# Optimization experiments

Hardware: AMD Instinct MI355X
Metric: run time of the kernel (lower is better)

The kernel has to match this reference:

```python
import jax, jax.numpy as jnp
import numpy as np

B, N, DF = 8, 4096, 768
K1, K2, DS = 8, 2, 128
KVQ, H, ITERS = 128, 1, 3
DH = KVQ // H
EPS_SA = 1e-8
SCALE = DH ** -0.5


def layer_norm(x, g, b, eps=1e-5):
    m = jnp.mean(x, axis=-1, keepdims=True)
    v = jnp.var(x, axis=-1, keepdims=True)
    return (x - m) / jnp.sqrt(v + eps) * g + b


def gru_cell(x, h, Wih, Whh, bih, bhh):
    gi = x @ Wih.T + bih
    gh = h @ Whh.T + bhh
    ir, iz, inn = jnp.split(gi, 3, axis=-1)
    hr, hz, hn = jnp.split(gh, 3, axis=-1)
    r = jax.nn.sigmoid(ir + hr)
    z = jax.nn.sigmoid(iz + hz)
    n = jnp.tanh(inn + r * hn)
    return (1.0 - z) * n + z * h


def setup_inputs() -> dict:
    key = jax.random.key(0)
    ks = jax.random.split(key, 24)
    s = 0.02
    f32 = jnp.float32
    return {
        'tokens': jax.random.normal(ks[0], (B, N, DF), f32),
        'parent_slots': jax.random.normal(ks[1], (B, K1, DS), f32),
        'parent_masks': jax.random.uniform(ks[2], (B, K1, N), f32),
        'eps_noise': jax.random.normal(ks[3], (B, K1, K2, DS), f32),
        'ln_in_g': jnp.ones((DF,), f32), 'ln_in_b': jnp.zeros((DF,), f32),
        'ln_s_g': jnp.ones((DS,), f32), 'ln_s_b': jnp.zeros((DS,), f32),
        'Wq': jax.random.normal(ks[4], (KVQ, DS), f32) * s,
        'Wk': jax.random.normal(ks[5], (KVQ, DF), f32) * s,
        'Wv': jax.random.normal(ks[6], (KVQ, DF), f32) * s,
        'gru_Wih': jax.random.normal(ks[7], (3 * DS, KVQ), f32) * s,
        'gru_Whh': jax.random.normal(ks[8], (3 * DS, DS), f32) * s,
        'gru_bih': jnp.zeros((3 * DS,), f32),
        'gru_bhh': jnp.zeros((3 * DS,), f32),
        'mlp_ln_g': jnp.ones((DS,), f32), 'mlp_ln_b': jnp.zeros((DS,), f32),
        'mlp_W1': jax.random.normal(ks[9], (4 * DS, DS), f32) * s,
        'mlp_b1': jnp.zeros((4 * DS,), f32),
        'mlp_W2': jax.random.normal(ks[10], (DS, 4 * DS), f32) * s,
        'mlp_b2': jnp.zeros((DS,), f32),
    }


def reference(tokens, parent_slots, parent_masks, eps_noise,
              ln_in_g, ln_in_b, ln_s_g, ln_s_b, Wq, Wk, Wv,
              gru_Wih, gru_Whh, gru_bih, gru_bhh,
              mlp_ln_g, mlp_ln_b, mlp_W1, mlp_b1, mlp_W2, mlp_b2):
    BK = B * K1
    # parent-mask gating (all parents vectorized, folded into batch)
    denom = jnp.mean(parent_masks, axis=-1, keepdims=True)          # [B,K1,1]
    safe = (denom > 1e-6).astype(tokens.dtype)
    w_scaled = safe * (parent_masks / (denom + 1e-6)) + (1.0 - safe)  # [B,K1,N]
    tg = (tokens[:, None, :, :] * w_scaled[..., None]).reshape(BK, N, DF)
    slots = (parent_slots[:, :, None, :] + 0.01 * eps_noise).reshape(BK, K2, DS)

    inp = layer_norm(tg, ln_in_g, ln_in_b)
    k = (inp @ Wk.T).reshape(BK, N, H, DH)
    v = (inp @ Wv.T).reshape(BK, N, H, DH)

    attn_bw = None
    for _ in range(ITERS):
        slots_prev = slots
        sn = layer_norm(slots, ln_s_g, ln_s_b)
        q = (sn @ Wq.T).reshape(BK, K2, H, DH)
        dots = jnp.einsum('bihd,bjhd->bihj', q, k) * SCALE          # [BK,K2,H,N]
        attn = jax.nn.softmax(dots, axis=1) + EPS_SA                # softmax over slots
        attn_bw = attn
        attn_w = attn / jnp.sum(attn, axis=-1, keepdims=True)
        updates = jnp.einsum('bjhd,bihj->bihd', v, attn_w).reshape(BK * K2, KVQ)
        slots = gru_cell(updates, slots_prev.reshape(BK * K2, DS),
                         gru_Wih, gru_Whh, gru_bih, gru_bhh).reshape(BK, K2, DS)
        h = layer_norm(slots, mlp_ln_g, mlp_ln_b)
        slots = jax.nn.gelu(h @ mlp_W1.T + mlp_b1, approximate=False) @ mlp_W2.T + mlp_b2

    attn_out = jnp.mean(attn_bw, axis=2)                            # [BK,K2,N]
    child_objects = slots.reshape(B, K1 * K2, DS)
    child_gating = (attn_out.reshape(B, K1, K2, N) * parent_masks[:, :, None, :]).reshape(B, K1 * K2, N)
    return child_objects, child_gating
```

## Files before the change

### kernel.cpp

```cpp
#include <hip/hip_runtime.h>
#include <math.h>

#define SCALE_ 0.08838834764831843f

typedef __attribute__((ext_vector_type(8))) short bf16x8;
typedef __attribute__((ext_vector_type(4))) float f32x4;
typedef __attribute__((ext_vector_type(8))) unsigned short u16x8;

static const size_t OFF_VAR   = 0;
static const size_t OFF_DENOM = 32768;
static const size_t OFF_GSUM  = 32832;
static const size_t OFF_BIAS  = 33088;
static const size_t OFF_QKB   = 33344;
static const size_t OFF_SSUM  = 33472;
static const size_t OFF_SLOTS = 33600;
static const size_t OFF_Q     = 49984;
static const size_t OFF_U     = 66368;
static const size_t OFF_WQBF  = 82752;
static const size_t OFF_WIHBF = 90944;
static const size_t OFF_WHHBF = 115520;
static const size_t OFF_W1BF  = 140096;
static const size_t OFF_WM2BF = 172864;
static const size_t OFF_WKVBF = 205632;
static const size_t OFF_KVB   = 303936;

__device__ __forceinline__ float wred64(float v) {
#pragma unroll
  for (int off = 32; off > 0; off >>= 1) v += __shfl_xor(v, off, 64);
  return v;
}

__device__ __forceinline__ unsigned short f2bf(float f) {
  unsigned u = __float_as_uint(f);
  unsigned r = (u + 0x7fffu + ((u >> 16) & 1u)) >> 16;
  return (unsigned short)r;
}

__device__ __forceinline__ unsigned pack2(float a, float b) {
  return (unsigned)f2bf(a) | ((unsigned)f2bf(b) << 16);
}

__device__ __forceinline__ float bf2f(unsigned short s) {
  return __uint_as_float((unsigned)s << 16);
}

__global__ __launch_bounds__(256) void prep_all_k(
    const float* __restrict__ Wk, const float* __restrict__ Wv,
    const float* __restrict__ g, const float* __restrict__ bb,
    const float* __restrict__ Wq, const float* __restrict__ Wih,
    const float* __restrict__ Whh, const float* __restrict__ W1,
    const float* __restrict__ W2, const float* __restrict__ pm,
    unsigned short* __restrict__ wkv, float* __restrict__ gsum,
    float* __restrict__ biasArr,
    unsigned short* __restrict__ Wqbf, unsigned short* __restrict__ Wihbf,
    unsigned short* __restrict__ Whhbf, unsigned short* __restrict__ W1bf,
    unsigned short* __restrict__ Wm2bf, float* __restrict__ denomArr)
{
  __shared__ float red4[4];
  int bi = blockIdx.x, t = threadIdx.x;
  if (bi < 64) {
    int j = bi*4 + (t >> 6), lane = t & 63;
    const float* w = (j < 128) ? (Wk + (size_t)j*768) : (Wv + (size_t)(j-128)*768);
    float gs = 0.f, bs = 0.f;
    int key = j & 7;
#pragma unroll
    for (int s = 0; s < 12; ++s) {
      int dd = lane + s*64;
      float wv = w[dd], gv = g[dd];
      gs += gv*wv; bs += bb[dd]*wv;
      int sw = (dd & ~63) | (((((dd >> 3) & 7) ^ key)) << 3) | (dd & 7);
      wkv[(size_t)j*768 + sw] = f2bf(wv*gv);
    }
    gs = wred64(gs); bs = wred64(bs);
    if (lane == 0) { gsum[j] = gs; biasArr[j] = bs; }
  } else if (bi < 128) {
    int idx = (bi-64)*256 + t;  Wqbf[idx]  = f2bf(Wq[idx]);
  } else if (bi < 320) {
    int idx = (bi-128)*256 + t; Wihbf[idx] = f2bf(Wih[idx]);
  } else if (bi < 512) {
    int idx = (bi-320)*256 + t; Whhbf[idx] = f2bf(Whh[idx]);
  } else if (bi < 768) {
    int idx = (bi-512)*256 + t; W1bf[idx]  = f2bf(W1[idx]);
  } else if (bi < 1024) {
    int idx = (bi-768)*256 + t; Wm2bf[idx] = f2bf(W2[idx]);
  } else {
    int bk = bi - 1024;
    float s = 0.f;
#pragma unroll
    for (int k = 0; k < 16; ++k) s += pm[bk*4096 + t + k*256];
    s = wred64(s);
    if ((t & 63) == 0) red4[t >> 6] = s;
    __syncthreads();
    if (t == 0) denomArr[bk] = (red4[0]+red4[1]+red4[2]+red4[3])*(1.f/4096.f);
  }
}

__global__ __launch_bounds__(256) void gemm_kv_k(
    const float* __restrict__ tokens, const unsigned short* __restrict__ wkv,
    const float* __restrict__ gsum, unsigned short* __restrict__ KVb,
    float* __restrict__ varArr)
{
  __shared__ unsigned short As[64*64];
  __shared__ unsigned short Bs[256*64];
  __shared__ float meanS[64];
  int r0 = blockIdx.x*64;
  int t = threadIdx.x;
  int w = t >> 6, lane = t & 63;
  int lm = lane & 15, lq = lane >> 4;
  int g16 = t >> 4, seg = t & 15;
  int m0 = (w >> 1)*32, n0 = (w & 1)*128;

  f32x4 acc[2][8];
#pragma unroll
  for (int a = 0; a < 2; ++a)
#pragma unroll
    for (int c = 0; c < 8; ++c) acc[a][c] = f32x4{0.f, 0.f, 0.f, 0.f};
  float s1[4] = {0.f,0.f,0.f,0.f}, s2[4] = {0.f,0.f,0.f,0.f};

  for (int k0 = 0; k0 < 768; k0 += 64) {
    __syncthreads();
#pragma unroll
    for (int s = 0; s < 8; ++s) {
      int row = w*64 + s*8;
      __builtin_amdgcn_global_load_lds(
        (const __attribute__((address_space(1))) void*)
          (wkv + (size_t)(row + (lane >> 3))*768 + k0 + (lane & 7)*8),
        (__attribute__((address_space(3))) void*)(&Bs[row*64]), 16, 0, 0);
    }
#pragma unroll
    for (int p = 0; p < 4; ++p) {
      int row = p*16 + g16;
      float4 x = *(const float4*)(tokens + (size_t)(r0 + row)*768 + k0 + seg*4);
      s1[p] += x.x + x.y + x.z + x.w;
      s2[p] += x.x*x.x + x.y*x.y + x.z*x.z + x.w*x.w;
      int off = row*64 + (((seg >> 1) ^ (row & 7)) << 3) + (seg & 1)*4;
      *(uint2*)(&As[off]) = make_uint2(pack2(x.x, x.y), pack2(x.z, x.w));
    }
    __syncthreads();
#pragma unroll
    for (int kk8 = 0; kk8 < 8; kk8 += 4) {
      bf16x8 af[2], bfr[8];
#pragma unroll
      for (int mt = 0; mt < 2; ++mt) {
        int row = m0 + mt*16 + lm;
        af[mt] = *(const bf16x8*)(&As[row*64 + (((kk8 + lq) ^ (row & 7)) << 3)]);
      }
#pragma unroll
      for (int nt = 0; nt < 8; ++nt) {
        int row = n0 + nt*16 + lm;
        bfr[nt] = *(const bf16x8*)(&Bs[row*64 + (((kk8 + lq) ^ (row & 7)) << 3)]);
      }
#pragma unroll
      for (int mt = 0; mt < 2; ++mt)
#pragma unroll
        for (int nt = 0; nt < 8; ++nt)
          acc[mt][nt] = __builtin_amdgcn_mfma_f32_16x16x32_bf16(
              af[mt], bfr[nt], acc[mt][nt], 0, 0, 0);
    }
  }
#pragma unroll
  for (int p = 0; p < 4; ++p) {
#pragma unroll
    for (int m = 8; m >= 1; m >>= 1) {
      s1[p] += __shfl_xor(s1[p], m, 16);
      s2[p] += __shfl_xor(s2[p], m, 16);
    }
  }
  if (seg == 0) {
#pragma unroll
    for (int p = 0; p < 4; ++p) {
      int row = p*16 + g16;
      float m = s1[p]*(1.f/768.f);
      meanS[row] = m;
      varArr[r0 + row] = s2[p]*(1.f/768.f) - m*m;
    }
  }
  __syncthreads();
#pragma unroll
  for (int nt = 0; nt < 8; ++nt) {
    int jg = n0 + nt*16 + lm;
    float gs = gsum[jg];
#pragma unroll
    for (int mt = 0; mt < 2; ++mt) {
#pragma unroll
      for (int reg = 0; reg < 4; ++reg) {
        int rl = m0 + mt*16 + lq*4 + reg;
        KVb[(size_t)(r0 + rl)*256 + jg] = f2bf(acc[mt][nt][reg] - meanS[rl]*gs);
      }
    }
  }
}

__global__ __launch_bounds__(256, 1) void slots_init_q_k(
    const float* __restrict__ ps, const float* __restrict__ eps,
    const float* __restrict__ g_s, const float* __restrict__ b_s,
    const unsigned short* __restrict__ Wqbf, const float* __restrict__ biasArr,
    float* __restrict__ slots, float* __restrict__ qg, float* __restrict__ qkb,
    float* __restrict__ Ssum, float* __restrict__ U)
{
  __shared__ unsigned short Fsn[2048];
  __shared__ float qkbL[16];
  int R0 = blockIdx.x*16;
  int t = threadIdx.x;
  int w = t >> 6, ln = t & 63, lm = ln & 15, lq = ln >> 4;
  if (t < 16) qkbL[t] = 0.f;
  {
    int r = t >> 4, dseg = t & 15, ds8 = dseg*8;
    int row = R0 + r, bk = row >> 1;
    float xv[8]; float s1 = 0.f, s2 = 0.f;
#pragma unroll
    for (int j = 0; j < 8; ++j) {
      int d = ds8 + j;
      float x = ps[bk*128 + d] + 0.01f*eps[row*128 + d];
      slots[row*128 + d] = x;
      U[row*128 + d] = 0.f;
      xv[j] = x; s1 += x; s2 += x*x;
    }
#pragma unroll
    for (int m = 8; m >= 1; m >>= 1) {
      s1 += __shfl_xor(s1, m, 16);
      s2 += __shfl_xor(s2, m, 16);
    }
    float mean = s1*(1.f/128.f);
    float var = s2*(1.f/128.f) - mean*mean;
    float rstd = rsqrtf(var + 1e-5f);
    float sv[8];
#pragma unroll
    for (int j = 0; j < 8; ++j) {
      int d = ds8 + j;
      sv[j] = (xv[j] - mean)*rstd*g_s[d] + b_s[d];
    }
    int fa = ((dseg >> 2)*64 + (dseg & 3)*16 + r)*8;
    *(uint4*)&Fsn[fa] = make_uint4(pack2(sv[0],sv[1]), pack2(sv[2],sv[3]),
                                   pack2(sv[4],sv[5]), pack2(sv[6],sv[7]));
  }
  __syncthreads();
  {
    bf16x8 af[4];
#pragma unroll
    for (int kc = 0; kc < 4; ++kc)
      af[kc] = *(const bf16x8*)(&Fsn[(kc*64 + ln)*8]);
    float pr[4] = {0.f, 0.f, 0.f, 0.f};
#pragma unroll
    for (int i = 0; i < 2; ++i) {
      int n0 = w*32 + i*16;
      f32x4 acc = f32x4{0.f,0.f,0.f,0.f};
#pragma unroll
      for (int kc = 0; kc < 4; ++kc) {
        bf16x8 bw = *(const bf16x8*)(&Wqbf[(size_t)(n0+lm)*128 + kc*32 + lq*8]);
        acc = __builtin_amdgcn_mfma_f32_16x16x32_bf16(af[kc], bw, acc, 0,0,0);
      }
      int n = n0 + lm;
      float bk_ = biasArr[n];
#pragma unroll
      for (int reg = 0; reg < 4; ++reg) {
        int row = lq*4 + reg;
        qg[(size_t)(R0 + row)*128 + n] = acc[reg];
        pr[reg] += acc[reg]*bk_;
      }
    }
#pragma unroll
    for (int reg = 0; reg < 4; ++reg) {
#pragma unroll
      for (int m = 8; m >= 1; m >>= 1) pr[reg] += __shfl_xor(pr[reg], m, 16);
    }
    if (lm == 0) {
#pragma unroll
      for (int reg = 0; reg < 4; ++reg)
        atomicAdd(&qkbL[lq*4 + reg], pr[reg]);
    }
  }
  __syncthreads();
  if (t < 16) { qkb[R0 + t] = qkbL[t]; Ssum[R0 + t] = 0.f; }
}

__global__ __launch_bounds__(256) void attn_fused_k(
    const unsigned short* __restrict__ KVb, const float* __restrict__ qg,
    const float* __restrict__ qkb, const float* __restrict__ varArr,
    const float* __restrict__ denomArr, const float* __restrict__ pm,
    float* __restrict__ U, float* __restrict__ Ssum,
    float* __restrict__ outG, int last)
{
  __shared__ float KVs[32*260];
  __shared__ float qs[2048];
  __shared__ float was[16*33];
  __shared__ float qkbs[16];
  int bi = blockIdx.x;
  int b = bi & 7, ch = bi >> 3;
  int t = threadIdx.x;
#pragma unroll
  for (int s = 0; s < 2; ++s)
    ((float4*)qs)[s*256 + t] = ((const float4*)(qg + b*2048))[s*256 + t];
  if (t < 16) qkbs[t] = qkb[b*16 + t];
  int p = t >> 5, nl = t & 31;
  int iu = t >> 4, dg = t & 15;
  int bk = b*8 + p;
  float den = denomArr[bk];
  float acc8[8];
#pragma unroll
  for (int j = 0; j < 8; ++j) acc8[j] = 0.f;
  float sA0 = 0.f, sA1 = 0.f;
  const float* q0 = qs + (p*2)*128;
  const float* q1 = q0 + 128;
  __syncthreads();
  float qb0 = qkbs[p*2], qb1 = qkbs[p*2 + 1];
  for (int sub = 0; sub < 4; ++sub) {
    int n0 = ch*128 + sub*32;
    if (sub) __syncthreads();
    {
      int nn = t >> 3, jj = t & 7;
#pragma unroll
      for (int s = 0; s < 4; ++s) {
        int col8 = jj + s*8;
        u16x8 kv8 = *(const u16x8*)&KVb[((size_t)(b*4096 + n0 + nn))*256 + col8*8];
        float4 f0, f1;
        f0.x = bf2f(kv8[0]); f0.y = bf2f(kv8[1]); f0.z = bf2f(kv8[2]); f0.w = bf2f(kv8[3]);
        f1.x = bf2f(kv8[4]); f1.y = bf2f(kv8[5]); f1.z = bf2f(kv8[6]); f1.w = bf2f(kv8[7]);
        *(float4*)&KVs[nn*260 + col8*8] = f0;
        *(float4*)&KVs[nn*260 + col8*8 + 4] = f1;
      }
    }
    __syncthreads();
    float d0 = 0.f, d1 = 0.f;
    const float* kr = KVs + nl*260;
#pragma unroll 8
    for (int j4 = 0; j4 < 32; ++j4) {
      float4 kv = *(const float4*)(kr + j4*4);
      float4 qa = *(const float4*)(q0 + j4*4);
      float4 qb = *(const float4*)(q1 + j4*4);
      d0 += kv.x*qa.x + kv.y*qa.y + kv.z*qa.z + kv.w*qa.w;
      d1 += kv.x*qb.x + kv.y*qb.y + kv.z*qb.z + kv.w*qb.w;
    }
    int n = n0 + nl;
    float pmv = pm[(size_t)bk*4096 + n];
    float c = (den > 1e-6f) ? (pmv/(den + 1e-6f)) : 1.f;
    float vv = varArr[b*4096 + n];
    float al = c*rsqrtf(c*c*vv + 1e-5f);
    float dd0 = SCALE_*(al*d0 + qb0);
    float dd1 = SCALE_*(al*d1 + qb1);
    float mx = fmaxf(dd0, dd1);
    float e0 = expf(dd0 - mx), e1 = expf(dd1 - mx);
    float inv = 1.f/(e0 + e1);
    float o0 = e0*inv + 1e-8f;
    float o1 = e1*inv + 1e-8f;
    sA0 += o0; sA1 += o1;
    was[(p*2)*33 + nl] = o0*al;
    was[(p*2 + 1)*33 + nl] = o1*al;
    if (last) {
      outG[((size_t)(bk*2))*4096 + n] = o0*pmv;
      outG[((size_t)(bk*2 + 1))*4096 + n] = o1*pmv;
    }
    __syncthreads();
    const float* vb = KVs + 128 + dg*8;
    const float* wr = was + iu*33;
#pragma unroll 8
    for (int nn = 0; nn < 32; ++nn) {
      float wv = wr[nn];
      float4 v0 = *(const float4*)(vb + nn*260);
      float4 v1 = *(const float4*)(vb + nn*260 + 4);
      acc8[0] += wv*v0.x; acc8[1] += wv*v0.y; acc8[2] += wv*v0.z; acc8[3] += wv*v0.w;
      acc8[4] += wv*v1.x; acc8[5] += wv*v1.y; acc8[6] += wv*v1.z; acc8[7] += wv*v1.w;
    }
  }
#pragma unroll
  for (int m = 16; m >= 1; m >>= 1) {
    sA0 += __shfl_xor(sA0, m, 32);
    sA1 += __shfl_xor(sA1, m, 32);
  }
  if (nl == 0) {
    atomicAdd(&Ssum[bk*2], sA0);
    atomicAdd(&Ssum[bk*2 + 1], sA1);
  }
  float* ur = U + (size_t)(b*16 + iu)*128 + dg*8;
#pragma unroll
  for (int j = 0; j < 8; ++j) atomicAdd(ur + j, acc8[j]);
}

__global__ __launch_bounds__(256, 1) void gru_mlp_q_k(
    const float* __restrict__ Uin, const float* __restrict__ Ssum,
    const float* __restrict__ biasArr,
    const unsigned short* __restrict__ Wihbf, const unsigned short* __restrict__ Whhbf,
    const float* __restrict__ bih, const float* __restrict__ bhh,
    const float* __restrict__ mlp_g, const float* __restrict__ mlp_b,
    const unsigned short* __restrict__ W1bf, const float* __restrict__ b1,
    const unsigned short* __restrict__ Wm2bf, const float* __restrict__ b2,
    const float* __restrict__ ln_s_g, const float* __restrict__ ln_s_b,
    const unsigned short* __restrict__ Wqbf,
    float* __restrict__ slots, float* __restrict__ qg, float* __restrict__ qkb,
    float* __restrict__ SsumW, float* __restrict__ Uw,
    float* __restrict__ outObj, int last)
{
  __shared__ unsigned short FXx[2048], FXh[2048], Fhn[2048], Fsn[2048];
  __shared__ unsigned short Ft1[8192];
  __shared__ float G_rz[16*256];
  __shared__ float G_in[16*128];
  __shared__ float G_hn[16*128];
  __shared__ float hs_[16*128];
  __shared__ float os_[16*128];
  __shared__ float qkbL[16];

  int R0 = blockIdx.x*16;
  int t = threadIdx.x;
  int w = t >> 6, ln = t & 63;
  int lm = ln & 15, lq = ln >> 4;

  {
    int r = t >> 4, dseg = t & 15, ds8 = dseg*8;
    int R = R0 + r;
    const float* up = Uin + (size_t)R*128 + ds8;
    float4 u0 = *(const float4*)(up);
    float4 u1 = *(const float4*)(up + 4);
    float Sv = 1.f/Ssum[R];
    float4 bv0 = *(const float4*)(biasArr + 128 + ds8);
    float4 bv1 = *(const float4*)(biasArr + 132 + ds8);
    float xv[8];
    xv[0]=u0.x*Sv+bv0.x; xv[1]=u0.y*Sv+bv0.y; xv[2]=u0.z*Sv+bv0.z; xv[3]=u0.w*Sv+bv0.w;
    xv[4]=u1.x*Sv+bv1.x; xv[5]=u1.y*Sv+bv1.y; xv[6]=u1.z*Sv+bv1.z; xv[7]=u1.w*Sv+bv1.w;
    if (!last) {
      *(float4*)(Uw + (size_t)R*128 + ds8) = make_float4(0.f,0.f,0.f,0.f);
      *(float4*)(Uw + (size_t)R*128 + ds8 + 4) = make_float4(0.f,0.f,0.f,0.f);
    }
    float4 h0 = *(const float4*)(slots + (size_t)R*128 + ds8);
    float4 h1 = *(const float4*)(slots + (size_t)R*128 + ds8 + 4);
    *(float4*)(hs_ + r*128 + ds8) = h0;
    *(float4*)(hs_ + r*128 + ds8 + 4) = h1;
    int fa = ((dseg >> 2)*64 + (dseg & 3)*16 + r)*8;
    *(uint4*)&FXx[fa] = make_uint4(pack2(xv[0],xv[1]), pack2(xv[2],xv[3]),
                                   pack2(xv[4],xv[5]), pack2(xv[6],xv[7]));
    *(uint4*)&FXh[fa] = make_uint4(pack2(h0.x,h0.y), pack2(h0.z,h0.w),
                                   pack2(h1.x,h1.y), pack2(h1.z,h1.w));
    if (t < 16) qkbL[t] = 0.f;
  }
  __syncthreads();

  {
    bf16x8 ax[4], ah[4];
#pragma unroll
    for (int kc = 0; kc < 4; ++kc) {
      ax[kc] = *(const bf16x8*)(&FXx[(kc*64 + ln)*8]);
      ah[kc] = *(const bf16x8*)(&FXh[(kc*64 + ln)*8]);
    }
    if (w < 2) {
#pragma unroll
      for (int i = 0; i < 8; ++i) {
        int n0 = (w*8 + i)*16;
        f32x4 acc = f32x4{0.f,0.f,0.f,0.f};
#pragma unroll
        for (int kc = 0; kc < 4; ++kc) {
          bf16x8 bi_ = *(const bf16x8*)(&Wihbf[(size_t)(n0+lm)*128 + kc*32 + lq*8]);
          acc = __builtin_amdgcn_mfma_f32_16x16x32_bf16(ax[kc], bi_, acc, 0,0,0);
        }
#pragma unroll
        for (int kc = 0; kc < 4; ++kc) {
          bf16x8 bh_ = *(const bf16x8*)(&Whhbf[(size_t)(n0+lm)*128 + kc*32 + lq*8]);
          acc = __builtin_amdgcn_mfma_f32_16x16x32_bf16(ah[kc], bh_, acc, 0,0,0);
        }
#pragma unroll
        for (int reg = 0; reg < 4; ++reg)
          G_rz[(lq*4+reg)*256 + n0 + lm] = acc[reg];
      }
    } else if (w == 2) {
#pragma unroll
      for (int i = 0; i < 8; ++i) {
        int n0 = 256 + i*16;
        f32x4 acc = f32x4{0.f,0.f,0.f,0.f};
#pragma unroll
        for (int kc = 0; kc < 4; ++kc) {
          bf16x8 bi_ = *(const bf16x8*)(&Wihbf[(size_t)(n0+lm)*128 + kc*32 + lq*8]);
          acc = __builtin_amdgcn_mfma_f32_16x16x32_bf16(ax[kc], bi_, acc, 0,0,0);
        }
#pragma unroll
        for (int reg = 0; reg < 4; ++reg)
          G_in[(lq*4+reg)*128 + i*16 + lm] = acc[reg];
      }
    } else {
#pragma unroll
      for (int i = 0; i < 8; ++i) {
        int n0 = 256 + i*16;
        f32x4 acc = f32x4{0.f,0.f,0.f,0.f};
#pragma unroll
        for (int kc = 0; kc < 4; ++kc) {
          bf16x8 bh_ = *(const bf16x8*)(&Whhbf[(size_t)(n0+lm)*128 + kc*32 + lq*8]);
          acc = __builtin_amdgcn_mfma_f32_16x16x32_bf16(ah[kc], bh_, acc, 0,0,0);
        }
#pragma unroll
        for (int reg = 0; reg < 4; ++reg)
          G_hn[(lq*4+reg)*128 + i*16 + lm] = acc[reg];
      }
    }
  }
  __syncthreads();

  {
    int r = t >> 4, dseg = t & 15, ds8 = dseg*8;
    float hp[8];
    float s1 = 0.f, s2 = 0.f;
#pragma unroll
    for (int j = 0; j < 8; ++j) {
      int d = ds8 + j;
      float rg = G_rz[r*256 + d] + bih[d] + bhh[d];
      float zg = G_rz[r*256 + 128 + d] + bih[128+d] + bhh[128+d];
      float ing = G_in[r*128 + d] + bih[256+d];
      float hng = G_hn[r*128 + d] + bhh[256+d];
      float rv = 1.f/(1.f + expf(-rg));
      float zv = 1.f/(1.f + expf(-zg));
      float nv = tanhf(ing + rv*hng);
      float h0 = hs_[r*128 + d];
      float h = (1.f - zv)*nv + zv*h0;
      hp[j] = h;
      s1 += h; s2 += h*h;
    }
#pragma unroll
    for (int m = 8; m >= 1; m >>= 1) {
      s1 += __shfl_xor(s1, m, 16);
      s2 += __shfl_xor(s2, m, 16);
    }
    float mean = s1*(1.f/128.f);
    float var = s2*(1.f/128.f) - mean*mean;
    float rstd = rsqrtf(var + 1e-5f);
    float hv[8];
#pragma unroll
    for (int j = 0; j < 8; ++j) {
      int d = ds8 + j;
      hv[j] = (hp[j] - mean)*rstd*mlp_g[d] + mlp_b[d];
    }
    int fa = ((dseg >> 2)*64 + (dseg & 3)*16 + r)*8;
    *(uint4*)&Fhn[fa] = make_uint4(pack2(hv[0],hv[1]), pack2(hv[2],hv[3]),
                                   pack2(hv[4],hv[5]), pack2(hv[6],hv[7]));
  }
  __syncthreads();

  {
    bf16x8 af[4];
#pragma unroll
    for (int kc = 0; kc < 4; ++kc)
      af[kc] = *(const bf16x8*)(&Fhn[(kc*64 + ln)*8]);
#pragma unroll
    for (int i = 0; i < 8; ++i) {
      int n0 = (w*8 + i)*16;
      f32x4 acc = f32x4{0.f,0.f,0.f,0.f};
#pragma unroll
      for (int kc = 0; kc < 4; ++kc) {
        bf16x8 bw = *(const bf16x8*)(&W1bf[(size_t)(n0+lm)*128 + kc*32 + lq*8]);
        acc = __builtin_amdgcn_mfma_f32_16x16x32_bf16(af[kc], bw, acc, 0,0,0);
      }
      int kdim = n0 + lm;
      float bb = b1[kdim];
      int kc2 = kdim >> 5;
      int sub = (kdim >> 3) & 3;
      int jj = kdim & 7;
#pragma unroll
      for (int reg = 0; reg < 4; ++reg) {
        float v = acc[reg] + bb;
        float gel = 0.5f*v*(1.f + erff(v*0.70710678118654752f));
        Ft1[(kc2*64 + sub*16 + lq*4 + reg)*8 + jj] = f2bf(gel);
      }
    }
  }
  __syncthreads();

  {
#pragma unroll
    for (int i = 0; i < 2; ++i) {
      int n0 = w*32 + i*16;
      f32x4 acc = f32x4{0.f,0.f,0.f,0.f};
#pragma unroll
      for (int kc = 0; kc < 16; ++kc) {
        bf16x8 af = *(const bf16x8*)(&Ft1[(kc*64 + ln)*8]);
        bf16x8 bw = *(const bf16x8*)(&Wm2bf[(size_t)(n0+lm)*512 + kc*32 + lq*8]);
        acc = __builtin_amdgcn_mfma_f32_16x16x32_bf16(af, bw, acc, 0,0,0);
      }
      int n = n0 + lm;
      float bb = b2[n];
#pragma unroll
      for (int reg = 0; reg < 4; ++reg) {
        int row = lq*4 + reg;
        float o = acc[reg] + bb;
        slots[(size_t)(R0 + row)*128 + n] = o;
        os_[row*128 + n] = o;
        if (last) outObj[(size_t)(R0 + row)*128 + n] = o;
      }
    }
  }

  if (last) return;

  __syncthreads();
  {
    int r = t >> 4, dseg = t & 15, ds8 = dseg*8;
    float ov[8];
    float s1 = 0.f, s2 = 0.f;
#pragma unroll
    for (int j = 0; j < 8; ++j) {
      float o = os_[r*128 + ds8 + j];
      ov[j] = o; s1 += o; s2 += o*o;
    }
#pragma unroll
    for (int m = 8; m >= 1; m >>= 1) {
      s1 += __shfl_xor(s1, m, 16);
      s2 += __shfl_xor(s2, m, 16);
    }
    float mean = s1*(1.f/128.f);
    float var = s2*(1.f/128.f) - mean*mean;
    float rstd = rsqrtf(var + 1e-5f);
    float sv[8];
#pragma unroll
    for (int j = 0; j < 8; ++j) {
      int d = ds8 + j;
      sv[j] = (ov[j] - mean)*rstd*ln_s_g[d] + ln_s_b[d];
    }
    int fa = ((dseg >> 2)*64 + (dseg & 3)*16 + r)*8;
    *(uint4*)&Fsn[fa] = make_uint4(pack2(sv[0],sv[1]), pack2(sv[2],sv[3]),
                                   pack2(sv[4],sv[5]), pack2(sv[6],sv[7]));
  }
  __syncthreads();

  {
    bf16x8 af[4];
#pragma unroll
    for (int kc = 0; kc < 4; ++kc)
      af[kc] = *(const bf16x8*)(&Fsn[(kc*64 + ln)*8]);
    float pr[4] = {0.f, 0.f, 0.f, 0.f};
#pragma unroll
    for (int i = 0; i < 2; ++i) {
      int n0 = w*32 + i*16;
      f32x4 acc = f32x4{0.f,0.f,0.f,0.f};
#pragma unroll
      for (int kc = 0; kc < 4; ++kc) {
        bf16x8 bw = *(const bf16x8*)(&Wqbf[(size_t)(n0+lm)*128 + kc*32 + lq*8]);
        acc = __builtin_amdgcn_mfma_f32_16x16x32_bf16(af[kc], bw, acc, 0,0,0);
      }
      int n = n0 + lm;
      float bk_ = biasArr[n];
#pragma unroll
      for (int reg = 0; reg < 4; ++reg) {
        int row = lq*4 + reg;
        qg[(size_t)(R0 + row)*128 + n] = acc[reg];
        pr[reg] += acc[reg]*bk_;
      }
    }
#pragma unroll
    for (int reg = 0; reg < 4; ++reg) {
#pragma unroll
      for (int m = 8; m >= 1; m >>= 1) pr[reg] += __shfl_xor(pr[reg], m, 16);
    }
    if (lm == 0) {
#pragma unroll
      for (int reg = 0; reg < 4; ++reg)
        atomicAdd(&qkbL[lq*4 + reg], pr[reg]);
    }
  }
  __syncthreads();
  if (t < 16) {
    qkb[R0 + t] = qkbL[t];
    SsumW[R0 + t] = 0.f;
  }
}

extern "C" void kernel_launch(void* const* d_in, const int* in_sizes, int n_in,
                              void* d_out, int out_size, void* d_ws, size_t ws_size,
                              hipStream_t stream) {
  const float* tokens = (const float*)d_in[0];
  const float* pslots = (const float*)d_in[1];
  const float* pmasks = (const float*)d_in[2];
  const float* eps    = (const float*)d_in[3];
  const float* ln_in_g= (const float*)d_in[4];
  const float* ln_in_b= (const float*)d_in[5];
  const float* ln_s_g = (const float*)d_in[6];
  const float* ln_s_b = (const float*)d_in[7];
  const float* Wq     = (const float*)d_in[8];
  const float* Wk     = (const float*)d_in[9];
  const float* Wv     = (const float*)d_in[10];
  const float* Wih    = (const float*)d_in[11];
  const float* Whh    = (const float*)d_in[12];
  const float* bih    = (const float*)d_in[13];
  const float* bhh    = (const float*)d_in[14];
  const float* mlp_g  = (const float*)d_in[15];
  const float* mlp_b  = (const float*)d_in[16];
  const float* W1     = (const float*)d_in[17];
  const float* b1     = (const float*)d_in[18];
  const float* W2     = (const float*)d_in[19];
  const float* b2     = (const float*)d_in[20];
  float* ws  = (float*)d_ws;
  float* out = (float*)d_out;
  unsigned short* wkvbf = (unsigned short*)(ws + OFF_WKVBF);
  unsigned short* wqbf  = (unsigned short*)(ws + OFF_WQBF);
  unsigned short* wihbf = (unsigned short*)(ws + OFF_WIHBF);
  unsigned short* whhbf = (unsigned short*)(ws + OFF_WHHBF);
  unsigned short* w1bf  = (unsigned short*)(ws + OFF_W1BF);
  unsigned short* wm2bf = (unsigned short*)(ws + OFF_WM2BF);
  unsigned short* kvb   = (unsigned short*)(ws + OFF_KVB);

  prep_all_k<<<1088, 256, 0, stream>>>(Wk, Wv, ln_in_g, ln_in_b,
                                       Wq, Wih, Whh, W1, W2, pmasks,
                                       wkvbf, ws + OFF_GSUM, ws + OFF_BIAS,
                                       wqbf, wihbf, whhbf, w1bf, wm2bf,
                                       ws + OFF_DENOM);
  gemm_kv_k<<<512, 256, 0, stream>>>(tokens, wkvbf, ws + OFF_GSUM,
                                     kvb, ws + OFF_VAR);
  slots_init_q_k<<<8, 256, 0, stream>>>(pslots, eps, ln_s_g, ln_s_b,
                                        wqbf, ws + OFF_BIAS,
                                        ws + OFF_SLOTS, ws + OFF_Q,
                                        ws + OFF_QKB, ws + OFF_SSUM,
                                        ws + OFF_U);
  for (int it = 0; it < 3; ++it) {
    int last = (it == 2);
    attn_fused_k<<<256, 256, 0, stream>>>(kvb, ws + OFF_Q, ws + OFF_QKB,
                                          ws + OFF_VAR, ws + OFF_DENOM, pmasks,
                                          ws + OFF_U, ws + OFF_SSUM,
                                          out + 16384, last);
    gru_mlp_q_k<<<8, 256, 0, stream>>>(ws + OFF_U, ws + OFF_SSUM,
                                       ws + OFF_BIAS, wihbf, whhbf, bih, bhh,
                                       mlp_g, mlp_b, w1bf, b1, wm2bf, b2,
                                       ln_s_g, ln_s_b, wqbf,
                                       ws + OFF_SLOTS, ws + OFF_Q, ws + OFF_QKB,
                                       ws + OFF_SSUM, ws + OFF_U, out, last);
  }
}
```

Before: 397.8 us.

## Double-buffer KV GEMM with register A fragments; replace U atomics with partial sums

```diff
diff --git a/kernel.cpp b/kernel.cpp
--- a/kernel.cpp
+++ b/kernel.cpp
@@ -15,14 +15,14 @@
 static const size_t OFF_SSUM  = 33472;
 static const size_t OFF_SLOTS = 33600;
 static const size_t OFF_Q     = 49984;
-static const size_t OFF_U     = 66368;
-static const size_t OFF_WQBF  = 82752;
-static const size_t OFF_WIHBF = 90944;
-static const size_t OFF_WHHBF = 115520;
-static const size_t OFF_W1BF  = 140096;
-static const size_t OFF_WM2BF = 172864;
-static const size_t OFF_WKVBF = 205632;
-static const size_t OFF_KVB   = 303936;
+static const size_t OFF_WQBF  = 66368;
+static const size_t OFF_WIHBF = 74560;
+static const size_t OFF_WHHBF = 99136;
+static const size_t OFF_W1BF  = 123712;
+static const size_t OFF_WM2BF = 156480;
+static const size_t OFF_WKVBF = 189248;
+static const size_t OFF_UPART = 287552;
+static const size_t OFF_KVB   = 811840;
 
 __device__ __forceinline__ float wred64(float v) {
 #pragma unroll
@@ -62,14 +62,12 @@
     int j = bi*4 + (t >> 6), lane = t & 63;
     const float* w = (j < 128) ? (Wk + (size_t)j*768) : (Wv + (size_t)(j-128)*768);
     float gs = 0.f, bs = 0.f;
-    int key = j & 7;
 #pragma unroll
     for (int s = 0; s < 12; ++s) {
       int dd = lane + s*64;
       float wv = w[dd], gv = g[dd];
       gs += gv*wv; bs += bb[dd]*wv;
-      int sw = (dd & ~63) | (((((dd >> 3) & 7) ^ key)) << 3) | (dd & 7);
-      wkv[(size_t)j*768 + sw] = f2bf(wv*gv);
+      wkv[(size_t)j*768 + dd] = f2bf(wv*gv);
     }
     gs = wred64(gs); bs = wred64(bs);
     if (lane == 0) { gsum[j] = gs; biasArr[j] = bs; }
@@ -95,98 +93,98 @@
   }
 }
 
+#define DMA_B(kstep, buf) \
+  { int k0_ = (kstep)*32; \
+    _Pragma("unroll") \
+    for (int s_ = 0; s_ < 4; ++s_) { \
+      int nb_ = w*64 + s_*16; \
+      __builtin_amdgcn_global_load_lds( \
+        (const __attribute__((address_space(1))) void*) \
+          (wkv + (size_t)(nb_ + nrow)*768 + k0_ + gsw*8), \
+        (__attribute__((address_space(3))) void*)(Bs + (buf)*8192 + nb_*32), \
+        16, 0, 0); \
+    } }
+
 __global__ __launch_bounds__(256) void gemm_kv_k(
     const float* __restrict__ tokens, const unsigned short* __restrict__ wkv,
     const float* __restrict__ gsum, unsigned short* __restrict__ KVb,
     float* __restrict__ varArr)
 {
-  __shared__ unsigned short As[64*64];
-  __shared__ unsigned short Bs[256*64];
-  __shared__ float meanS[64];
+  __shared__ unsigned short Bs[2*8192];
   int r0 = blockIdx.x*64;
   int t = threadIdx.x;
   int w = t >> 6, lane = t & 63;
   int lm = lane & 15, lq = lane >> 4;
-  int g16 = t >> 4, seg = t & 15;
-  int m0 = (w >> 1)*32, n0 = (w & 1)*128;
-
-  f32x4 acc[2][8];
-#pragma unroll
-  for (int a = 0; a < 2; ++a)
-#pragma unroll
-    for (int c = 0; c < 8; ++c) acc[a][c] = f32x4{0.f, 0.f, 0.f, 0.f};
-  float s1[4] = {0.f,0.f,0.f,0.f}, s2[4] = {0.f,0.f,0.f,0.f};
-
-  for (int k0 = 0; k0 < 768; k0 += 64) {
-    __syncthreads();
-#pragma unroll
-    for (int s = 0; s < 8; ++s) {
-      int row = w*64 + s*8;
-      __builtin_amdgcn_global_load_lds(
-        (const __attribute__((address_space(1))) void*)
-          (wkv + (size_t)(row + (lane >> 3))*768 + k0 + (lane & 7)*8),
-        (__attribute__((address_space(3))) void*)(&Bs[row*64]), 16, 0, 0);
-    }
-#pragma unroll
-    for (int p = 0; p < 4; ++p) {
-      int row = p*16 + g16;
-      float4 x = *(const float4*)(tokens + (size_t)(r0 + row)*768 + k0 + seg*4);
-      s1[p] += x.x + x.y + x.z + x.w;
-      s2[p] += x.x*x.x + x.y*x.y + x.z*x.z + x.w*x.w;
-      int off = row*64 + (((seg >> 1) ^ (row & 7)) << 3) + (seg & 1)*4;
-      *(uint2*)(&As[off]) = make_uint2(pack2(x.x, x.y), pack2(x.z, x.w));
-    }
-    __syncthreads();
-#pragma unroll
-    for (int kk8 = 0; kk8 < 8; kk8 += 4) {
-      bf16x8 af[2], bfr[8];
-#pragma unroll
-      for (int mt = 0; mt < 2; ++mt) {
-        int row = m0 + mt*16 + lm;
-        af[mt] = *(const bf16x8*)(&As[row*64 + (((kk8 + lq) ^ (row & 7)) << 3)]);
-      }
-#pragma unroll
-      for (int nt = 0; nt < 8; ++nt) {
-        int row = n0 + nt*16 + lm;
-        bfr[nt] = *(const bf16x8*)(&Bs[row*64 + (((kk8 + lq) ^ (row & 7)) << 3)]);
-      }
-#pragma unroll
-      for (int mt = 0; mt < 2; ++mt)
-#pragma unroll
-        for (int nt = 0; nt < 8; ++nt)
-          acc[mt][nt] = __builtin_amdgcn_mfma_f32_16x16x32_bf16(
-              af[mt], bfr[nt], acc[mt][nt], 0, 0, 0);
-    }
-  }
-#pragma unroll
-  for (int p = 0; p < 4; ++p) {
-#pragma unroll
-    for (int m = 8; m >= 1; m >>= 1) {
-      s1[p] += __shfl_xor(s1[p], m, 16);
-      s2[p] += __shfl_xor(s2[p], m, 16);
-    }
-  }
-  if (seg == 0) {
-#pragma unroll
-    for (int p = 0; p < 4; ++p) {
-      int row = p*16 + g16;
-      float m = s1[p]*(1.f/768.f);
-      meanS[row] = m;
-      varArr[r0 + row] = s2[p]*(1.f/768.f) - m*m;
-    }
-  }
-  __syncthreads();
-#pragma unroll
-  for (int nt = 0; nt < 8; ++nt) {
-    int jg = n0 + nt*16 + lm;
-    float gs = gsum[jg];
-#pragma unroll
-    for (int mt = 0; mt < 2; ++mt) {
-#pragma unroll
-      for (int reg = 0; reg < 4; ++reg) {
-        int rl = m0 + mt*16 + lq*4 + reg;
-        KVb[(size_t)(r0 + rl)*256 + jg] = f2bf(acc[mt][nt][reg] - meanS[rl]*gs);
-      }
+  int nrow = lane >> 2;
+  int gsw = (lane & 3) ^ ((lane >> 3) & 3);
+  int nswz = lq ^ ((lm >> 1) & 3);
+
+  const float* aptr = tokens + (size_t)(r0 + w*16 + lm)*768 + lq*8;
+
+  f32x4 acc[16];
+#pragma unroll
+  for (int c = 0; c < 16; ++c) acc[c] = f32x4{0.f, 0.f, 0.f, 0.f};
+  float s1 = 0.f, s2 = 0.f;
+
+  float4 A0[2], A1[2];
+  DMA_B(0, 0);
+  A0[0] = *(const float4*)(aptr);
+  A1[0] = *(const float4*)(aptr + 4);
+  DMA_B(1, 1);
+  __builtin_amdgcn_s_waitcnt(0x0F76);
+  __builtin_amdgcn_s_barrier();
+
+#pragma unroll
+  for (int k = 0; k < 24; ++k) {
+    const int kb = k & 1, kn = kb ^ 1;
+    float4 x0 = A0[kb], x1 = A1[kb];
+    s1 += x0.x + x0.y + x0.z + x0.w + x1.x + x1.y + x1.z + x1.w;
+    s2 += x0.x*x0.x + x0.y*x0.y + x0.z*x0.z + x0.w*x0.w
+        + x1.x*x1.x + x1.y*x1.y + x1.z*x1.z + x1.w*x1.w;
+    unsigned u0 = pack2(x0.x, x0.y), u1 = pack2(x0.z, x0.w);
+    unsigned u2 = pack2(x1.x, x1.y), u3 = pack2(x1.z, x1.w);
+    bf16x8 afrag;
+    { uint4 tmp = make_uint4(u0, u1, u2, u3);
+      afrag = *(bf16x8*)&tmp; }
+    if (k < 23) {
+      A0[kn] = *(const float4*)(aptr + (k+1)*32);
+      A1[kn] = *(const float4*)(aptr + (k+1)*32 + 4);
+    }
+    const unsigned short* bsr = Bs + kb*8192;
+#pragma unroll
+    for (int nt = 0; nt < 16; ++nt) {
+      bf16x8 bfr = *(const bf16x8*)(bsr + (nt*16 + lm)*32 + nswz*8);
+      acc[nt] = __builtin_amdgcn_mfma_f32_16x16x32_bf16(afrag, bfr, acc[nt], 0, 0, 0);
+    }
+    if (k < 23) {
+      __builtin_amdgcn_s_barrier();
+      if (k < 22) {
+        DMA_B(k+2, kb);
+        __builtin_amdgcn_s_waitcnt(0x0F76);
+      } else {
+        __builtin_amdgcn_s_waitcnt(0x0F72);
+      }
+      __builtin_amdgcn_s_barrier();
+    }
+  }
+
+  s1 += __shfl_xor(s1, 16, 64); s1 += __shfl_xor(s1, 32, 64);
+  s2 += __shfl_xor(s2, 16, 64); s2 += __shfl_xor(s2, 32, 64);
+  float mean = s1*(1.f/768.f);
+  float var  = s2*(1.f/768.f) - mean*mean;
+  if (lq == 0) varArr[r0 + w*16 + lm] = var;
+  float meanR[4];
+#pragma unroll
+  for (int reg = 0; reg < 4; ++reg)
+    meanR[reg] = __shfl(mean, lq*4 + reg, 64);
+#pragma unroll
+  for (int nt = 0; nt < 16; ++nt) {
+    int col = nt*16 + lm;
+    float gs = gsum[col];
+#pragma unroll
+    for (int reg = 0; reg < 4; ++reg) {
+      int row = r0 + w*16 + lq*4 + reg;
+      KVb[(size_t)row*256 + col] = f2bf(acc[nt][reg] - meanR[reg]*gs);
     }
   }
 }
@@ -196,7 +194,7 @@
     const float* __restrict__ g_s, const float* __restrict__ b_s,
     const unsigned short* __restrict__ Wqbf, const float* __restrict__ biasArr,
     float* __restrict__ slots, float* __restrict__ qg, float* __restrict__ qkb,
-    float* __restrict__ Ssum, float* __restrict__ U)
+    float* __restrict__ Ssum)
 {
   __shared__ unsigned short Fsn[2048];
   __shared__ float qkbL[16];
@@ -213,7 +211,6 @@
       int d = ds8 + j;
       float x = ps[bk*128 + d] + 0.01f*eps[row*128 + d];
       slots[row*128 + d] = x;
-      U[row*128 + d] = 0.f;
       xv[j] = x; s1 += x; s2 += x*x;
     }
 #pragma unroll
@@ -278,7 +275,7 @@
     const unsigned short* __restrict__ KVb, const float* __restrict__ qg,
     const float* __restrict__ qkb, const float* __restrict__ varArr,
     const float* __restrict__ denomArr, const float* __restrict__ pm,
-    float* __restrict__ U, float* __restrict__ Ssum,
+    float* __restrict__ Upart, float* __restrict__ Ssum,
     float* __restrict__ outG, int last)
 {
   __shared__ float KVs[32*260];
@@ -371,13 +368,13 @@
     atomicAdd(&Ssum[bk*2], sA0);
     atomicAdd(&Ssum[bk*2 + 1], sA1);
   }
-  float* ur = U + (size_t)(b*16 + iu)*128 + dg*8;
-#pragma unroll
-  for (int j = 0; j < 8; ++j) atomicAdd(ur + j, acc8[j]);
+  float* up = Upart + ((size_t)(bi*16 + iu))*128 + dg*8;
+  *(float4*)up = make_float4(acc8[0], acc8[1], acc8[2], acc8[3]);
+  *(float4*)(up + 4) = make_float4(acc8[4], acc8[5], acc8[6], acc8[7]);
 }
 
 __global__ __launch_bounds__(256, 1) void gru_mlp_q_k(
-    const float* __restrict__ Uin, const float* __restrict__ Ssum,
+    const float* __restrict__ Upart, const float* __restrict__ Ssum,
     const float* __restrict__ biasArr,
     const unsigned short* __restrict__ Wihbf, const unsigned short* __restrict__ Whhbf,
     const float* __restrict__ bih, const float* __restrict__ bhh,
@@ -387,8 +384,7 @@
     const float* __restrict__ ln_s_g, const float* __restrict__ ln_s_b,
     const unsigned short* __restrict__ Wqbf,
     float* __restrict__ slots, float* __restrict__ qg, float* __restrict__ qkb,
-    float* __restrict__ SsumW, float* __restrict__ Uw,
-    float* __restrict__ outObj, int last)
+    float* __restrict__ SsumW, float* __restrict__ outObj, int last)
 {
   __shared__ unsigned short FXx[2048], FXh[2048], Fhn[2048], Fsn[2048];
   __shared__ unsigned short Ft1[8192];
@@ -407,19 +403,23 @@
   {
     int r = t >> 4, dseg = t & 15, ds8 = dseg*8;
     int R = R0 + r;
-    const float* up = Uin + (size_t)R*128 + ds8;
-    float4 u0 = *(const float4*)(up);
-    float4 u1 = *(const float4*)(up + 4);
+    float ua[8];
+#pragma unroll
+    for (int j = 0; j < 8; ++j) ua[j] = 0.f;
+    const float* up = Upart + (size_t)R*128 + ds8;
+#pragma unroll
+    for (int ch = 0; ch < 32; ++ch) {
+      float4 u0 = *(const float4*)(up + (size_t)ch*16384);
+      float4 u1 = *(const float4*)(up + (size_t)ch*16384 + 4);
+      ua[0]+=u0.x; ua[1]+=u0.y; ua[2]+=u0.z; ua[3]+=u0.w;
+      ua[4]+=u1.x; ua[5]+=u1.y; ua[6]+=u1.z; ua[7]+=u1.w;
+    }
     float Sv = 1.f/Ssum[R];
     float4 bv0 = *(const float4*)(biasArr + 128 + ds8);
     float4 bv1 = *(const float4*)(biasArr + 132 + ds8);
     float xv[8];
-    xv[0]=u0.x*Sv+bv0.x; xv[1]=u0.y*Sv+bv0.y; xv[2]=u0.z*Sv+bv0.z; xv[3]=u0.w*Sv+bv0.w;
-    xv[4]=u1.x*Sv+bv1.x; xv[5]=u1.y*Sv+bv1.y; xv[6]=u1.z*Sv+bv1.z; xv[7]=u1.w*Sv+bv1.w;
-    if (!last) {
-      *(float4*)(Uw + (size_t)R*128 + ds8) = make_float4(0.f,0.f,0.f,0.f);
-      *(float4*)(Uw + (size_t)R*128 + ds8 + 4) = make_float4(0.f,0.f,0.f,0.f);
-    }
+    xv[0]=ua[0]*Sv+bv0.x; xv[1]=ua[1]*Sv+bv0.y; xv[2]=ua[2]*Sv+bv0.z; xv[3]=ua[3]*Sv+bv0.w;
+    xv[4]=ua[4]*Sv+bv1.x; xv[5]=ua[5]*Sv+bv1.y; xv[6]=ua[6]*Sv+bv1.z; xv[7]=ua[7]*Sv+bv1.w;
     float4 h0 = *(const float4*)(slots + (size_t)R*128 + ds8);
     float4 h1 = *(const float4*)(slots + (size_t)R*128 + ds8 + 4);
     *(float4*)(hs_ + r*128 + ds8) = h0;
@@ -701,19 +701,18 @@
   slots_init_q_k<<<8, 256, 0, stream>>>(pslots, eps, ln_s_g, ln_s_b,
                                         wqbf, ws + OFF_BIAS,
                                         ws + OFF_SLOTS, ws + OFF_Q,
-                                        ws + OFF_QKB, ws + OFF_SSUM,
-                                        ws + OFF_U);
+                                        ws + OFF_QKB, ws + OFF_SSUM);
   for (int it = 0; it < 3; ++it) {
     int last = (it == 2);
     attn_fused_k<<<256, 256, 0, stream>>>(kvb, ws + OFF_Q, ws + OFF_QKB,
                                           ws + OFF_VAR, ws + OFF_DENOM, pmasks,
-                                          ws + OFF_U, ws + OFF_SSUM,
+                                          ws + OFF_UPART, ws + OFF_SSUM,
                                           out + 16384, last);
-    gru_mlp_q_k<<<8, 256, 0, stream>>>(ws + OFF_U, ws + OFF_SSUM,
+    gru_mlp_q_k<<<8, 256, 0, stream>>>(ws + OFF_UPART, ws + OFF_SSUM,
                                        ws + OFF_BIAS, wihbf, whhbf, bih, bhh,
                                        mlp_g, mlp_b, w1bf, b1, wm2bf, b2,
                                        ln_s_g, ln_s_b, wqbf,
                                        ws + OFF_SLOTS, ws + OFF_Q, ws + OFF_QKB,
-                                       ws + OFF_SSUM, ws + OFF_U, out, last);
-  }
-}
+                                       ws + OFF_SSUM, out, last);
+  }
+}
```

New measurement: 380.3 us. -4.4%, faster.
